# Performance work log

Measured on AMD Instinct MI355X. Metric: run time of the kernel, lower is better.

Reference implementation:

```python
import jax, jax.numpy as jnp
import numpy as np

N, IN_DIM, HID, HEADS, OUT_DIM, E = 10000, 512, 256, 8, 5, 40000
NEG_SLOPE = 0.2


def _gatv2(x, src, dst, Wl, bl, Wr, br, att, bias, concat):
    # PyG GATv2Conv (share_weights=False, add_self_loops handled by caller):
    # message m_ij = alpha_ij * (Wl x_j);  e_ij = att . LeakyReLU(Wl x_j + Wr x_i)
    n = x.shape[0]
    H, C = att.shape
    hl = (x @ Wl + bl).reshape(n, H, C)  # source transform
    hr = (x @ Wr + br).reshape(n, H, C)  # target transform
    g = jax.nn.leaky_relu(hl[src] + hr[dst], negative_slope=NEG_SLOPE)  # [E,H,C]
    score = jnp.einsum('ehc,hc->eh', g, att)  # [E,H]
    # segment softmax over incoming edges of each destination node
    m = jax.ops.segment_max(score, dst, num_segments=n)
    a = jnp.exp(score - m[dst])
    denom = jax.ops.segment_sum(a, dst, num_segments=n)
    alpha = a / (denom[dst] + 1e-16)
    out = jax.ops.segment_sum(alpha[..., None] * hl[src], dst, num_segments=n)  # [N,H,C]
    if concat:
        return out.reshape(n, H * C) + bias
    return out.mean(axis=1) + bias


def setup_inputs() -> dict:
    key = jax.random.key(0)
    ks = list(jax.random.split(key, 32))
    p = lambda i, shape: (jax.random.normal(ks[i], shape, dtype=jnp.float32) * 0.02)
    d = {
        'x': jax.random.normal(ks[0], (N, IN_DIM), dtype=jnp.float32),
        'edge_index': jax.random.randint(ks[1], (2, E), 0, N, dtype=jnp.int64)
            if jax.config.jax_enable_x64 else
            jax.random.randint(ks[1], (2, E), 0, N).astype(jnp.int32),
        # layer 0: in -> H*C, concat
        'Wl0': p(2, (IN_DIM, HEADS * HID)), 'bl0': jnp.zeros((HEADS * HID,), jnp.float32),
        'Wr0': p(3, (IN_DIM, HEADS * HID)), 'br0': jnp.zeros((HEADS * HID,), jnp.float32),
        'att0': p(4, (HEADS, HID)), 'b0': jnp.zeros((HEADS * HID,), jnp.float32),
        # layer 1: H*C -> H*C, concat
        'Wl1': p(5, (HEADS * HID, HEADS * HID)), 'bl1': jnp.zeros((HEADS * HID,), jnp.float32),
        'Wr1': p(6, (HEADS * HID, HEADS * HID)), 'br1': jnp.zeros((HEADS * HID,), jnp.float32),
        'att1': p(7, (HEADS, HID)), 'b1': jnp.zeros((HEADS * HID,), jnp.float32),
        # layer 2: H*C -> C (mean over heads)
        'Wl2': p(8, (HEADS * HID, HEADS * HID)), 'bl2': jnp.zeros((HEADS * HID,), jnp.float32),
        'Wr2': p(9, (HEADS * HID, HEADS * HID)), 'br2': jnp.zeros((HEADS * HID,), jnp.float32),
        'att2': p(10, (HEADS, HID)), 'b2': jnp.zeros((HID,), jnp.float32),
        # heads
        'W_pam1': p(11, (HID, HID // 2)), 'b_pam1': jnp.zeros((HID // 2,), jnp.float32),
        'W_pam2': p(12, (HID // 2, OUT_DIM)), 'b_pam2': jnp.zeros((OUT_DIM,), jnp.float32),
        'W_sur1': p(13, (HID, HID // 2)), 'b_sur1': jnp.zeros((HID // 2,), jnp.float32),
        'W_sur2': p(14, (HID // 2, 1)), 'b_sur2': jnp.zeros((1,), jnp.float32),
    }
    return d


def reference(x, edge_index, Wl0, bl0, Wr0, br0, att0, b0,
              Wl1, bl1, Wr1, br1, att1, b1,
              Wl2, bl2, Wr2, br2, att2, b2,
              W_pam1, b_pam1, W_pam2, b_pam2,
              W_sur1, b_sur1, W_sur2, b_sur2):
    n = x.shape[0]
    loop = jnp.arange(n, dtype=edge_index.dtype)
    src = jnp.concatenate([edge_index[0], loop])  # add_self_loops=True
    dst = jnp.concatenate([edge_index[1], loop])
    h = _gatv2(x, src, dst, Wl0, bl0, Wr0, br0, att0, b0, concat=True)
    h = jax.nn.elu(h)  # dropout: eval mode -> identity
    h = _gatv2(h, src, dst, Wl1, bl1, Wr1, br1, att1, b1, concat=True)
    h = jax.nn.elu(h)
    h = _gatv2(h, src, dst, Wl2, bl2, Wr2, br2, att2, b2, concat=False)  # [N, HID]
    pam50 = jax.nn.relu(h @ W_pam1 + b_pam1) @ W_pam2 + b_pam2
    surv = jax.nn.relu(h @ W_sur1 + b_sur1) @ W_sur2 + b_sur2
    return pam50, surv
```

## Files before the change

kernel.cpp:

```cpp
#include <hip/hip_runtime.h>
#include <hip/hip_bf16.h>
#include <math.h>

#define IN_DIM 512
#define HID 256
#define HEADS 8
#define HC (HEADS * HID)
#define OUT_DIM 5
#define NEG_SLOPE 0.2f

typedef short s16x8 __attribute__((ext_vector_type(8)));
typedef float f32x4 __attribute__((ext_vector_type(4)));

__device__ inline unsigned short bf16_rne(float f) {
  unsigned u = __float_as_uint(f);
  unsigned r = (u + 0x7fffu + ((u >> 16) & 1u)) >> 16;
  return (unsigned short)r;
}
__device__ inline float bf16_to_f(unsigned short h) {
  return __uint_as_float(((unsigned)h) << 16);
}
__device__ inline void split8(const float* f, s16x8& hv, s16x8& lv) {
  s16x8 h, l;
#pragma unroll
  for (int i = 0; i < 8; i++) {
    unsigned short hs = bf16_rne(f[i]);
    h[i] = (short)hs;
    l[i] = (short)bf16_rne(f[i] - bf16_to_f(hs));
  }
  hv = h; lv = l;
}

__global__ void split_pad(const float* __restrict__ X,
                          unsigned short* __restrict__ hi,
                          unsigned short* __restrict__ lo, long ntotal) {
  long i = ((long)blockIdx.x * blockDim.x + threadIdx.x) * 4;
  if (i >= ntotal) return;
  float4 v = *(const float4*)(X + i);
  ushort4 h, l;
  h.x = bf16_rne(v.x); l.x = bf16_rne(v.x - bf16_to_f(h.x));
  h.y = bf16_rne(v.y); l.y = bf16_rne(v.y - bf16_to_f(h.y));
  h.z = bf16_rne(v.z); l.z = bf16_rne(v.z - bf16_to_f(h.z));
  h.w = bf16_rne(v.w); l.w = bf16_rne(v.w - bf16_to_f(h.w));
  *(ushort4*)(hi + i) = h;
  *(ushort4*)(lo + i) = l;
}

__global__ __launch_bounds__(256) void wsplit_t(
    const float* __restrict__ W, unsigned short* __restrict__ thi,
    unsigned short* __restrict__ tlo, int K, int N) {
  __shared__ float tile[32][33];
  int tx = threadIdx.x & 31, ty = threadIdx.x >> 5;
  int n0 = blockIdx.x * 32, k0 = blockIdx.y * 32;
#pragma unroll
  for (int r = 0; r < 4; r++) {
    int k = k0 + ty + r * 8;
    tile[ty + r * 8][tx] = W[(size_t)k * N + n0 + tx];
  }
  __syncthreads();
#pragma unroll
  for (int r = 0; r < 4; r++) {
    int n = n0 + ty + r * 8;
    float v = tile[tx][ty + r * 8];
    unsigned short h = bf16_rne(v);
    thi[(size_t)n * K + k0 + tx] = h;
    tlo[(size_t)n * K + k0 + tx] = bf16_rne(v - bf16_to_f(h));
  }
}

#define GL16(gp, lp) __builtin_amdgcn_global_load_lds( \
    (const __attribute__((address_space(1))) void*)(gp), \
    (__attribute__((address_space(3))) void*)(lp), 16, 0, 0)

__global__ __launch_bounds__(256, 4) void gemm_planes2(
    const unsigned short* __restrict__ Ahi, const unsigned short* __restrict__ Alo,
    const unsigned short* __restrict__ Bhi, const unsigned short* __restrict__ Blo,
    const float* __restrict__ bias, float* __restrict__ C,
    int M, int Nc, int K) {
  __shared__ __attribute__((aligned(16))) unsigned short ah_s[128 * 32];
  __shared__ __attribute__((aligned(16))) unsigned short al_s[128 * 32];
  __shared__ __attribute__((aligned(16))) unsigned short bh_s[128 * 32];
  __shared__ __attribute__((aligned(16))) unsigned short bl_s[128 * 32];

  const int tid = threadIdx.x;
  const int lane = tid & 63;
  const int w = tid >> 6;
  const int wr = w >> 1, wc = w & 1;

  int nwg = gridDim.x * gridDim.y;
  int wgid = blockIdx.y * gridDim.x + blockIdx.x;
  int qq = nwg >> 3, rr = nwg & 7, xcd = wgid & 7, lid = wgid >> 3;
  int nid = (xcd < rr) ? xcd * (qq + 1) + lid
                       : rr * (qq + 1) + (xcd - rr) * qq + lid;
  const int col0 = (nid % gridDim.x) * 128;
  const int row0 = (nid / gridDim.x) * 128;

  const int lr = lane >> 2;
  const int lk = (((lane & 3) ^ ((lane >> 3) & 3))) * 8;
  const unsigned short* gAh = Ahi + (size_t)(row0 + lr) * K + lk;
  const unsigned short* gAl = Alo + (size_t)(row0 + lr) * K + lk;
  const unsigned short* gBh = Bhi + (size_t)(col0 + lr) * K + lk;
  const unsigned short* gBl = Blo + (size_t)(col0 + lr) * K + lk;

  f32x4 acc[4][4];
#pragma unroll
  for (int i = 0; i < 4; i++)
#pragma unroll
    for (int j = 0; j < 4; j++) acc[i][j] = (f32x4){0.f, 0.f, 0.f, 0.f};

  const int fr = lane & 15;
  const int fq = lane >> 4;
  const int sfq = (fq ^ ((fr >> 1) & 3)) * 8;

  for (int k0 = 0; k0 < K; k0 += 32) {
    __syncthreads();
#pragma unroll
    for (int c2 = 0; c2 < 2; c2++) {
      int c = w * 2 + c2;
      size_t roff = (size_t)c * 16 * K + k0;
      GL16(gAh + roff, &ah_s[c * 512]);
      GL16(gAl + roff, &al_s[c * 512]);
      GL16(gBh + roff, &bh_s[c * 512]);
      GL16(gBl + roff, &bl_s[c * 512]);
    }
    __syncthreads();

    s16x8 ah[4], al[4], bh[4], bl[4];
#pragma unroll
    for (int i = 0; i < 4; i++) {
      int off = (wr * 64 + i * 16 + fr) * 32 + sfq;
      ah[i] = *(const s16x8*)&ah_s[off];
      al[i] = *(const s16x8*)&al_s[off];
    }
#pragma unroll
    for (int j = 0; j < 4; j++) {
      int off = (wc * 64 + j * 16 + fr) * 32 + sfq;
      bh[j] = *(const s16x8*)&bh_s[off];
      bl[j] = *(const s16x8*)&bl_s[off];
    }
#pragma unroll
    for (int i = 0; i < 4; i++)
#pragma unroll
      for (int j = 0; j < 4; j++) {
        acc[i][j] = __builtin_amdgcn_mfma_f32_16x16x32_bf16(ah[i], bh[j], acc[i][j], 0, 0, 0);
        acc[i][j] = __builtin_amdgcn_mfma_f32_16x16x32_bf16(ah[i], bl[j], acc[i][j], 0, 0, 0);
        acc[i][j] = __builtin_amdgcn_mfma_f32_16x16x32_bf16(al[i], bh[j], acc[i][j], 0, 0, 0);
      }
  }

#pragma unroll
  for (int j = 0; j < 4; j++) {
    int col = col0 + wc * 64 + j * 16 + fr;
    float bj = bias[col];
#pragma unroll
    for (int i = 0; i < 4; i++) {
      int rbase = row0 + wr * 64 + i * 16 + fq * 4;
#pragma unroll
      for (int r = 0; r < 4; r++) {
        int row = rbase + r;
        if (row < M) C[(size_t)row * Nc + col] = acc[i][j][r] + bj;
      }
    }
  }
}

#define BM 64
#define BN 64
#define BK 16

template <bool RELU>
__global__ __launch_bounds__(256) void gemm_bias(
    const float* __restrict__ A, const float* __restrict__ W,
    const float* __restrict__ bias, float* __restrict__ out,
    int M, int Nc, int K) {
  __shared__ float As[BK][BM + 1];
  __shared__ float Bs[BK][BN + 1];
  const int tid = threadIdx.x;
  const int tx = tid & 15;
  const int ty = tid >> 4;
  const int row0 = blockIdx.y * BM;
  const int col0 = blockIdx.x * BN;

  float acc[4][4] = {};

  for (int k0 = 0; k0 < K; k0 += BK) {
#pragma unroll
    for (int i = 0; i < 4; i++) {
      int idx = tid + i * 256;
      int m = idx >> 4;
      int kk = idx & 15;
      int gm = row0 + m;
      As[kk][m] = (gm < M) ? A[(size_t)gm * K + k0 + kk] : 0.f;
    }
#pragma unroll
    for (int i = 0; i < 4; i++) {
      int idx = tid + i * 256;
      int kk = idx >> 6;
      int nn = idx & 63;
      Bs[kk][nn] = W[(size_t)(k0 + kk) * Nc + col0 + nn];
    }
    __syncthreads();
#pragma unroll
    for (int kk = 0; kk < BK; kk++) {
      float a[4], b[4];
#pragma unroll
      for (int i = 0; i < 4; i++) a[i] = As[kk][ty * 4 + i];
#pragma unroll
      for (int j = 0; j < 4; j++) b[j] = Bs[kk][tx * 4 + j];
#pragma unroll
      for (int i = 0; i < 4; i++)
#pragma unroll
        for (int j = 0; j < 4; j++) acc[i][j] += a[i] * b[j];
    }
    __syncthreads();
  }

#pragma unroll
  for (int i = 0; i < 4; i++) {
    int gm = row0 + ty * 4 + i;
    if (gm >= M) continue;
#pragma unroll
    for (int j = 0; j < 4; j++) {
      int gn = col0 + tx * 4 + j;
      float v = acc[i][j] + bias[gn];
      if (RELU) v = fmaxf(v, 0.f);
      out[(size_t)gm * Nc + gn] = v;
    }
  }
}

__global__ void count_dst(const int* __restrict__ ei, int* __restrict__ cnt,
                          int E, int Et) {
  int t = blockIdx.x * blockDim.x + threadIdx.x;
  if (t >= Et) return;
  int d = (t < E) ? ei[E + t] : t - E;
  atomicAdd(&cnt[d], 1);
}

#define SCAN_T 1024
__global__ __launch_bounds__(SCAN_T) void scan_offsets(
    const int* __restrict__ cnt, int* __restrict__ row_off, int N) {
  __shared__ int ssum[SCAN_T];
  int t = threadIdx.x;
  int per = (N + SCAN_T - 1) / SCAN_T;
  int beg = t * per, end = min(beg + per, N);
  int s = 0;
  for (int i = beg; i < end; i++) s += cnt[i];
  ssum[t] = s;
  __syncthreads();
  for (int off = 1; off < SCAN_T; off <<= 1) {
    int v = (t >= off) ? ssum[t - off] : 0;
    __syncthreads();
    ssum[t] += v;
    __syncthreads();
  }
  int run = (t == 0) ? 0 : ssum[t - 1];
  for (int i = beg; i < end; i++) { row_off[i] = run; run += cnt[i]; }
  if (t == 0) row_off[N] = ssum[SCAN_T - 1];
}

__global__ void scatter_edges(const int* __restrict__ ei,
                              const int* __restrict__ row_off,
                              int* __restrict__ fill,
                              int* __restrict__ esrc, int E, int Et) {
  int t = blockIdx.x * blockDim.x + threadIdx.x;
  if (t >= Et) return;
  int s, d;
  if (t < E) { s = ei[t]; d = ei[E + t]; } else { s = t - E; d = s; }
  int pos = row_off[d] + atomicAdd(&fill[d], 1);
  esrc[pos] = s;
}

template <int MODE>
__global__ __launch_bounds__(256) void node_attn(
    const float* __restrict__ hl, const float* __restrict__ hr,
    const int* __restrict__ row_off, const int* __restrict__ esrc,
    const float* __restrict__ att, const float* __restrict__ bias,
    float* __restrict__ outf, unsigned short* __restrict__ Chi,
    unsigned short* __restrict__ Clo, int N) {
  __shared__ float red[HC];
  int n = blockIdx.x;
  int t = threadIdx.x;
  int h = t >> 5;
  int l = t & 31;
  int beg = row_off[n], end = row_off[n + 1];

  const f32x4* attp = (const f32x4*)(att + h * HID + l * 8);
  const f32x4 at0 = attp[0], at1 = attp[1];
  const f32x4* hrp = (const f32x4*)(hr + (size_t)n * HC + h * HID + l * 8);
  const f32x4 hr0 = hrp[0], hr1 = hrp[1];

  float m = -1e30f, s = 0.f;
  f32x4 a0 = {0.f, 0.f, 0.f, 0.f}, a1 = {0.f, 0.f, 0.f, 0.f};
  for (int j = beg; j < end; j++) {
    int src = esrc[j];
    const f32x4* p = (const f32x4*)(hl + (size_t)src * HC + h * HID + l * 8);
    f32x4 v0 = p[0], v1 = p[1];
    float sc = 0.f;
#pragma unroll
    for (int q = 0; q < 4; q++) {
      float g0 = v0[q] + hr0[q]; g0 = (g0 > 0.f) ? g0 : NEG_SLOPE * g0; sc += at0[q] * g0;
      float g1 = v1[q] + hr1[q]; g1 = (g1 > 0.f) ? g1 : NEG_SLOPE * g1; sc += at1[q] * g1;
    }
#pragma unroll
    for (int off = 16; off > 0; off >>= 1) sc += __shfl_xor(sc, off);
    float mn = fmaxf(m, sc);
    float fold = expf(m - mn);
    float e = expf(sc - mn);
    s = s * fold + e;
    a0 = a0 * fold + e * v0;
    a1 = a1 * fold + e * v1;
    m = mn;
  }
  float inv = 1.f / (s + 1e-16f);
  a0 *= inv;
  a1 *= inv;

  int cbase = h * HID + l * 8;
  if (MODE == 1) {
    float v[8];
#pragma unroll
    for (int q = 0; q < 4; q++) {
      float xx = a0[q] + bias[cbase + q];
      v[q] = (xx > 0.f) ? xx : (expf(xx) - 1.f);
    }
#pragma unroll
    for (int q = 0; q < 4; q++) {
      float xx = a1[q] + bias[cbase + 4 + q];
      v[4 + q] = (xx > 0.f) ? xx : (expf(xx) - 1.f);
    }
    s16x8 hv, lv;
    split8(v, hv, lv);
    *(s16x8*)&Chi[(size_t)n * HC + cbase] = hv;
    *(s16x8*)&Clo[(size_t)n * HC + cbase] = lv;
  } else {
#pragma unroll
    for (int q = 0; q < 4; q++) red[cbase + q] = a0[q];
#pragma unroll
    for (int q = 0; q < 4; q++) red[cbase + 4 + q] = a1[q];
    __syncthreads();
    int c = t;
    float sm = 0.f;
#pragma unroll
    for (int hh = 0; hh < HEADS; hh++) sm += red[hh * HID + c];
    outf[(size_t)n * HID + c] = 0.125f * sm + bias[c];
  }
}

__global__ void head_final(const float* __restrict__ hid,
                           const float* __restrict__ W,
                           const float* __restrict__ b,
                           float* __restrict__ out, int N, int K, int O) {
  int t = blockIdx.x * blockDim.x + threadIdx.x;
  if (t >= N * O) return;
  int n = t / O, j = t % O;
  float s = b[j];
  const float* hrow = hid + (size_t)n * K;
  for (int k = 0; k < K; k++) s += hrow[k] * W[(size_t)k * O + j];
  out[t] = s;
}

static inline void run_big_gemm(const unsigned short* Ahi, const unsigned short* Alo,
                                const float* W, unsigned short* Wthi, unsigned short* Wtlo,
                                const float* bias, float* out, int M, int Nc, int K,
                                hipStream_t stream) {
  dim3 tg(Nc / 32, K / 32);
  wsplit_t<<<tg, 256, 0, stream>>>(W, Wthi, Wtlo, K, Nc);
  dim3 grid(Nc / 128, (M + 127) / 128);
  gemm_planes2<<<grid, 256, 0, stream>>>(Ahi, Alo, Wthi, Wtlo, bias, out, M, Nc, K);
}

static inline void run_gemm_f32(const float* A, const float* W, const float* bias,
                                float* out, int M, int Nc, int K, bool relu,
                                hipStream_t stream) {
  dim3 grid((Nc + BN - 1) / BN, (M + BM - 1) / BM);
  if (relu)
    gemm_bias<true><<<grid, 256, 0, stream>>>(A, W, bias, out, M, Nc, K);
  else
    gemm_bias<false><<<grid, 256, 0, stream>>>(A, W, bias, out, M, Nc, K);
}

extern "C" void kernel_launch(void* const* d_in, const int* in_sizes, int n_in,
                              void* d_out, int out_size, void* d_ws, size_t ws_size,
                              hipStream_t stream) {
  const float* x   = (const float*)d_in[0];
  const int*   ei  = (const int*)d_in[1];
  const float* Wl0 = (const float*)d_in[2];  const float* bl0 = (const float*)d_in[3];
  const float* Wr0 = (const float*)d_in[4];  const float* br0 = (const float*)d_in[5];
  const float* att0= (const float*)d_in[6];  const float* b0  = (const float*)d_in[7];
  const float* Wl1 = (const float*)d_in[8];  const float* bl1 = (const float*)d_in[9];
  const float* Wr1 = (const float*)d_in[10]; const float* br1 = (const float*)d_in[11];
  const float* att1= (const float*)d_in[12]; const float* b1  = (const float*)d_in[13];
  const float* Wl2 = (const float*)d_in[14]; const float* bl2 = (const float*)d_in[15];
  const float* Wr2 = (const float*)d_in[16]; const float* br2 = (const float*)d_in[17];
  const float* att2= (const float*)d_in[18]; const float* b2  = (const float*)d_in[19];
  const float* W_pam1 = (const float*)d_in[20]; const float* b_pam1 = (const float*)d_in[21];
  const float* W_pam2 = (const float*)d_in[22]; const float* b_pam2 = (const float*)d_in[23];
  const float* W_sur1 = (const float*)d_in[24]; const float* b_sur1 = (const float*)d_in[25];
  const float* W_sur2 = (const float*)d_in[26]; const float* b_sur2 = (const float*)d_in[27];

  const int N  = in_sizes[0] / IN_DIM;
  const int E  = in_sizes[1] / 2;
  const int Et = E + N;

  char* p = (char*)d_ws;
  const size_t NF = (size_t)N * HC;
  float* bufA = (float*)p;                 p += NF * 4;
  float* bufB = (float*)p;                 p += NF * 4;
  unsigned short* Chi = (unsigned short*)p; p += NF * 2;
  unsigned short* Clo = (unsigned short*)p; p += NF * 2;
  unsigned short* Wthi = (unsigned short*)p; p += (size_t)HC * HC * 2;
  unsigned short* Wtlo = (unsigned short*)p; p += (size_t)HC * HC * 2;
  int* row_off = (int*)p;                  p += (size_t)(N + 1) * 4;
  int* esrc    = (int*)p;                  p += (size_t)Et * 4;
  int* cnt     = (int*)p;                  p += (size_t)N * 4;
  int* fill    = (int*)p;                  p += (size_t)N * 4;
  unsigned short* Xhi = Chi;
  unsigned short* Xlo = Xhi + (size_t)N * IN_DIM;
  float* hfin = (float*)Chi;
  float* hid  = (float*)Clo;

  float* out_pam = (float*)d_out;
  float* out_sur = out_pam + (size_t)N * OUT_DIM;

  hipMemsetAsync(cnt, 0, N * 4, stream);
  hipMemsetAsync(fill, 0, N * 4, stream);
  count_dst<<<(Et + 255) / 256, 256, 0, stream>>>(ei, cnt, E, Et);
  scan_offsets<<<1, SCAN_T, 0, stream>>>(cnt, row_off, N);
  scatter_edges<<<(Et + 255) / 256, 256, 0, stream>>>(ei, row_off, fill, esrc, E, Et);

  split_pad<<<(unsigned)(((long)N * IN_DIM / 4 + 255) / 256), 256, 0, stream>>>(
      x, Xhi, Xlo, (long)N * IN_DIM);
  run_big_gemm(Xhi, Xlo, Wl0, Wthi, Wtlo, bl0, bufA, N, HC, IN_DIM, stream);
  run_big_gemm(Xhi, Xlo, Wr0, Wthi, Wtlo, br0, bufB, N, HC, IN_DIM, stream);
  node_attn<1><<<N, 256, 0, stream>>>(bufA, bufB, row_off, esrc, att0, b0,
                                      nullptr, Chi, Clo, N);

  run_big_gemm(Chi, Clo, Wl1, Wthi, Wtlo, bl1, bufA, N, HC, HC, stream);
  run_big_gemm(Chi, Clo, Wr1, Wthi, Wtlo, br1, bufB, N, HC, HC, stream);
  node_attn<1><<<N, 256, 0, stream>>>(bufA, bufB, row_off, esrc, att1, b1,
                                      nullptr, Chi, Clo, N);

  run_big_gemm(Chi, Clo, Wl2, Wthi, Wtlo, bl2, bufA, N, HC, HC, stream);
  run_big_gemm(Chi, Clo, Wr2, Wthi, Wtlo, br2, bufB, N, HC, HC, stream);
  node_attn<0><<<N, 256, 0, stream>>>(bufA, bufB, row_off, esrc, att2, b2,
                                      hfin, nullptr, nullptr, N);

  run_gemm_f32(hfin, W_pam1, b_pam1, hid, N, HID / 2, HID, true, stream);
  head_final<<<(N * OUT_DIM + 255) / 256, 256, 0, stream>>>(hid, W_pam2, b_pam2, out_pam, N, HID / 2, OUT_DIM);
  run_gemm_f32(hfin, W_sur1, b_sur1, hid, N, HID / 2, HID, true, stream);
  head_final<<<(N + 255) / 256, 256, 0, stream>>>(hid, W_sur2, b_sur2, out_sur, N, HID / 2, 1);
}
```

Measured before the change: 1.688 ms.

## Fuse layer-0 Wl/Wr GEMMs into one wide GEMM, interleave hl/hr buffer, merge MLP heads

Layer 0 now splits both Wl0 and Wr0 into one stacked transposed weight and runs a single GEMM producing an interleaved [N, 2*HC] buffer holding hl and hr per row. Per-column bias selection handles the two halves. Layers 1 and 2 still run two GEMMs but write into the same interleaved layout. The two head MLP first layers are concatenated into one 256-wide GEMM, and launch bounds drop from 4 to 3 waves per SIMD. Goal: fewer launches and better row locality for the gathers in node_attn, at the cost of a strided output layout and a changed occupancy hint.

```diff
diff --git a/kernel.cpp b/kernel.cpp
--- a/kernel.cpp
+++ b/kernel.cpp
@@ -6,6 +6,7 @@
 #define HID 256
 #define HEADS 8
 #define HC (HEADS * HID)
+#define HCX (2 * HC)
 #define OUT_DIM 5
 #define NEG_SLOPE 0.2f
 
@@ -72,11 +73,11 @@
     (const __attribute__((address_space(1))) void*)(gp), \
     (__attribute__((address_space(3))) void*)(lp), 16, 0, 0)
 
-__global__ __launch_bounds__(256, 4) void gemm_planes2(
+__global__ __launch_bounds__(256, 3) void gemm_planes2(
     const unsigned short* __restrict__ Ahi, const unsigned short* __restrict__ Alo,
     const unsigned short* __restrict__ Bhi, const unsigned short* __restrict__ Blo,
-    const float* __restrict__ bias, float* __restrict__ C,
-    int M, int Nc, int K) {
+    const float* __restrict__ biasL, const float* __restrict__ biasR,
+    float* __restrict__ C, int M, int Nc, int ldC, int K, int halfN) {
   __shared__ __attribute__((aligned(16))) unsigned short ah_s[128 * 32];
   __shared__ __attribute__((aligned(16))) unsigned short al_s[128 * 32];
   __shared__ __attribute__((aligned(16))) unsigned short bh_s[128 * 32];
@@ -151,14 +152,14 @@
 #pragma unroll
   for (int j = 0; j < 4; j++) {
     int col = col0 + wc * 64 + j * 16 + fr;
-    float bj = bias[col];
+    float bj = (col < halfN) ? biasL[col] : biasR[col - halfN];
 #pragma unroll
     for (int i = 0; i < 4; i++) {
       int rbase = row0 + wr * 64 + i * 16 + fq * 4;
 #pragma unroll
       for (int r = 0; r < 4; r++) {
         int row = rbase + r;
-        if (row < M) C[(size_t)row * Nc + col] = acc[i][j][r] + bj;
+        if (row < M) C[(size_t)row * ldC + col] = acc[i][j][r] + bj;
       }
     }
   }
@@ -287,14 +288,14 @@
 
   const f32x4* attp = (const f32x4*)(att + h * HID + l * 8);
   const f32x4 at0 = attp[0], at1 = attp[1];
-  const f32x4* hrp = (const f32x4*)(hr + (size_t)n * HC + h * HID + l * 8);
+  const f32x4* hrp = (const f32x4*)(hr + (size_t)n * HCX + h * HID + l * 8);
   const f32x4 hr0 = hrp[0], hr1 = hrp[1];
 
   float m = -1e30f, s = 0.f;
   f32x4 a0 = {0.f, 0.f, 0.f, 0.f}, a1 = {0.f, 0.f, 0.f, 0.f};
   for (int j = beg; j < end; j++) {
     int src = esrc[j];
-    const f32x4* p = (const f32x4*)(hl + (size_t)src * HC + h * HID + l * 8);
+    const f32x4* p = (const f32x4*)(hl + (size_t)src * HCX + h * HID + l * 8);
     f32x4 v0 = p[0], v1 = p[1];
     float sc = 0.f;
 #pragma unroll
@@ -347,7 +348,15 @@
   }
 }
 
-__global__ void head_final(const float* __restrict__ hid,
+__global__ void cat_heads(const float* __restrict__ Wp, const float* __restrict__ Ws,
+                          const float* __restrict__ bp, const float* __restrict__ bs,
+                          float* __restrict__ Wcat, float* __restrict__ bcat) {
+  int r = blockIdx.x, c = threadIdx.x;
+  Wcat[r * 256 + c] = (c < 128) ? Wp[r * 128 + c] : Ws[r * 128 + (c - 128)];
+  if (r == 0) bcat[c] = (c < 128) ? bp[c] : bs[c - 128];
+}
+
+__global__ void head_final(const float* __restrict__ hid, int ldH, int off,
                            const float* __restrict__ W,
                            const float* __restrict__ b,
                            float* __restrict__ out, int N, int K, int O) {
@@ -355,29 +364,9 @@
   if (t >= N * O) return;
   int n = t / O, j = t % O;
   float s = b[j];
-  const float* hrow = hid + (size_t)n * K;
+  const float* hrow = hid + (size_t)n * ldH + off;
   for (int k = 0; k < K; k++) s += hrow[k] * W[(size_t)k * O + j];
   out[t] = s;
-}
-
-static inline void run_big_gemm(const unsigned short* Ahi, const unsigned short* Alo,
-                                const float* W, unsigned short* Wthi, unsigned short* Wtlo,
-                                const float* bias, float* out, int M, int Nc, int K,
-                                hipStream_t stream) {
-  dim3 tg(Nc / 32, K / 32);
-  wsplit_t<<<tg, 256, 0, stream>>>(W, Wthi, Wtlo, K, Nc);
-  dim3 grid(Nc / 128, (M + 127) / 128);
-  gemm_planes2<<<grid, 256, 0, stream>>>(Ahi, Alo, Wthi, Wtlo, bias, out, M, Nc, K);
-}
-
-static inline void run_gemm_f32(const float* A, const float* W, const float* bias,
-                                float* out, int M, int Nc, int K, bool relu,
-                                hipStream_t stream) {
-  dim3 grid((Nc + BN - 1) / BN, (M + BM - 1) / BM);
-  if (relu)
-    gemm_bias<true><<<grid, 256, 0, stream>>>(A, W, bias, out, M, Nc, K);
-  else
-    gemm_bias<false><<<grid, 256, 0, stream>>>(A, W, bias, out, M, Nc, K);
 }
 
 extern "C" void kernel_launch(void* const* d_in, const int* in_sizes, int n_in,
@@ -405,8 +394,7 @@
 
   char* p = (char*)d_ws;
   const size_t NF = (size_t)N * HC;
-  float* bufA = (float*)p;                 p += NF * 4;
-  float* bufB = (float*)p;                 p += NF * 4;
+  float* bufAB = (float*)p;                 p += NF * 2 * 4;
   unsigned short* Chi = (unsigned short*)p; p += NF * 2;
   unsigned short* Clo = (unsigned short*)p; p += NF * 2;
   unsigned short* Wthi = (unsigned short*)p; p += (size_t)HC * HC * 2;
@@ -415,6 +403,8 @@
   int* esrc    = (int*)p;                  p += (size_t)Et * 4;
   int* cnt     = (int*)p;                  p += (size_t)N * 4;
   int* fill    = (int*)p;                  p += (size_t)N * 4;
+  float* Wcat  = (float*)p;                p += 256 * 256 * 4;
+  float* bcat  = (float*)p;                p += 256 * 4;
   unsigned short* Xhi = Chi;
   unsigned short* Xlo = Xhi + (size_t)N * IN_DIM;
   float* hfin = (float*)Chi;
@@ -422,32 +412,63 @@
 
   float* out_pam = (float*)d_out;
   float* out_sur = out_pam + (size_t)N * OUT_DIM;
+
+  float* hlp = bufAB;
+  float* hrp = bufAB + HC;
 
   hipMemsetAsync(cnt, 0, N * 4, stream);
   hipMemsetAsync(fill, 0, N * 4, stream);
   count_dst<<<(Et + 255) / 256, 256, 0, stream>>>(ei, cnt, E, Et);
   scan_offsets<<<1, SCAN_T, 0, stream>>>(cnt, row_off, N);
   scatter_edges<<<(Et + 255) / 256, 256, 0, stream>>>(ei, row_off, fill, esrc, E, Et);
+  cat_heads<<<256, 256, 0, stream>>>(W_pam1, W_sur1, b_pam1, b_sur1, Wcat, bcat);
 
   split_pad<<<(unsigned)(((long)N * IN_DIM / 4 + 255) / 256), 256, 0, stream>>>(
       x, Xhi, Xlo, (long)N * IN_DIM);
-  run_big_gemm(Xhi, Xlo, Wl0, Wthi, Wtlo, bl0, bufA, N, HC, IN_DIM, stream);
-  run_big_gemm(Xhi, Xlo, Wr0, Wthi, Wtlo, br0, bufB, N, HC, IN_DIM, stream);
-  node_attn<1><<<N, 256, 0, stream>>>(bufA, bufB, row_off, esrc, att0, b0,
+  {
+    dim3 tg(HC / 32, IN_DIM / 32);
+    wsplit_t<<<tg, 256, 0, stream>>>(Wl0, Wthi, Wtlo, IN_DIM, HC);
+    wsplit_t<<<tg, 256, 0, stream>>>(Wr0, Wthi + (size_t)HC * IN_DIM,
+                                     Wtlo + (size_t)HC * IN_DIM, IN_DIM, HC);
+    dim3 grid(HCX / 128, (N + 127) / 128);
+    gemm_planes2<<<grid, 256, 0, stream>>>(Xhi, Xlo, Wthi, Wtlo, bl0, br0,
+                                           bufAB, N, HCX, HCX, IN_DIM, HC);
+  }
+  node_attn<1><<<N, 256, 0, stream>>>(hlp, hrp, row_off, esrc, att0, b0,
                                       nullptr, Chi, Clo, N);
 
-  run_big_gemm(Chi, Clo, Wl1, Wthi, Wtlo, bl1, bufA, N, HC, HC, stream);
-  run_big_gemm(Chi, Clo, Wr1, Wthi, Wtlo, br1, bufB, N, HC, HC, stream);
-  node_attn<1><<<N, 256, 0, stream>>>(bufA, bufB, row_off, esrc, att1, b1,
+  {
+    dim3 tg(HC / 32, HC / 32);
+    dim3 grid(HC / 128, (N + 127) / 128);
+    wsplit_t<<<tg, 256, 0, stream>>>(Wl1, Wthi, Wtlo, HC, HC);
+    gemm_planes2<<<grid, 256, 0, stream>>>(Chi, Clo, Wthi, Wtlo, bl1, bl1,
+                                           bufAB, N, HC, HCX, HC, HC);
+    wsplit_t<<<tg, 256, 0, stream>>>(Wr1, Wthi, Wtlo, HC, HC);
+    gemm_planes2<<<grid, 256, 0, stream>>>(Chi, Clo, Wthi, Wtlo, br1, br1,
+                                           bufAB + HC, N, HC, HCX, HC, HC);
+  }
+  node_attn<1><<<N, 256, 0, stream>>>(hlp, hrp, row_off, esrc, att1, b1,
                                       nullptr, Chi, Clo, N);
 
-  run_big_gemm(Chi, Clo, Wl2, Wthi, Wtlo, bl2, bufA, N, HC, HC, stream);
-  run_big_gemm(Chi, Clo, Wr2, Wthi, Wtlo, br2, bufB, N, HC, HC, stream);
-  node_attn<0><<<N, 256, 0, stream>>>(bufA, bufB, row_off, esrc, att2, b2,
+  {
+    dim3 tg(HC / 32, HC / 32);
+    dim3 grid(HC / 128, (N + 127) / 128);
+    wsplit_t<<<tg, 256, 0, stream>>>(Wl2, Wthi, Wtlo, HC, HC);
+    gemm_planes2<<<grid, 256, 0, stream>>>(Chi, Clo, Wthi, Wtlo, bl2, bl2,
+                                           bufAB, N, HC, HCX, HC, HC);
+    wsplit_t<<<tg, 256, 0, stream>>>(Wr2, Wthi, Wtlo, HC, HC);
+    gemm_planes2<<<grid, 256, 0, stream>>>(Chi, Clo, Wthi, Wtlo, br2, br2,
+                                           bufAB + HC, N, HC, HCX, HC, HC);
+  }
+  node_attn<0><<<N, 256, 0, stream>>>(hlp, hrp, row_off, esrc, att2, b2,
                                       hfin, nullptr, nullptr, N);
 
-  run_gemm_f32(hfin, W_pam1, b_pam1, hid, N, HID / 2, HID, true, stream);
-  head_final<<<(N * OUT_DIM + 255) / 256, 256, 0, stream>>>(hid, W_pam2, b_pam2, out_pam, N, HID / 2, OUT_DIM);
-  run_gemm_f32(hfin, W_sur1, b_sur1, hid, N, HID / 2, HID, true, stream);
-  head_final<<<(N + 255) / 256, 256, 0, stream>>>(hid, W_sur2, b_sur2, out_sur, N, HID / 2, 1);
-}
+  {
+    dim3 grid(256 / BN, (N + BM - 1) / BM);
+    gemm_bias<true><<<grid, 256, 0, stream>>>(hfin, Wcat, bcat, hid, N, 256, HID);
+  }
+  head_final<<<(N * OUT_DIM + 255) / 256, 256, 0, stream>>>(
+      hid, 256, 0, W_pam2, b_pam2, out_pam, N, HID / 2, OUT_DIM);
+  head_final<<<(N + 255) / 256, 256, 0, stream>>>(
+      hid, 256, 128, W_sur2, b_sur2, out_sur, N, HID / 2, 1);
+}
```

Measured after the change: 1.573 ms. 6.8% less time.
